# Kernel optimization log

Measured on AMD Instinct MI355X. Metric: run time of the kernel, lower is better.

## Reference

```python
import jax, jax.numpy as jnp
import numpy as np

N_NODES = 50000
N_EDGES = 800000
IN_DIM = 128
OUT_DIM = 128
N_CLASSES = 10
N_GRAPHS = 64


def setup_inputs() -> dict:
    key = jax.random.key(0)
    ks = jax.random.split(key, 8)
    features = jax.random.normal(ks[0], (N_NODES, IN_DIM), dtype=jnp.float32)
    src = jax.random.randint(ks[1], (N_EDGES,), 0, N_NODES, dtype=jnp.int64)
    dst = jax.random.randint(ks[2], (N_EDGES,), 0, N_NODES, dtype=jnp.int64)
    graph_ids = jnp.sort(jax.random.randint(ks[3], (N_NODES,), 0, N_GRAPHS, dtype=jnp.int64))
    # GraphConv params (glorot-ish scale) and linear head params
    W = jax.random.normal(ks[4], (IN_DIM, OUT_DIM), dtype=jnp.float32) / np.sqrt(IN_DIM)
    b = jnp.zeros((OUT_DIM,), dtype=jnp.float32)
    W_head = jax.random.normal(ks[5], (OUT_DIM, N_CLASSES), dtype=jnp.float32) / np.sqrt(OUT_DIM)
    b_head = jnp.zeros((N_CLASSES,), dtype=jnp.float32)
    return {"features": features, "src": src, "dst": dst, "graph_ids": graph_ids,
            "W": W, "b": b, "W_head": W_head, "b_head": b_head}


def reference(features, src, dst, graph_ids, W, b, W_head, b_head):
    # DGL GraphConv, norm='both': D_out^-1/2 -> sum aggregate -> D_in^-1/2 -> XW+b -> relu
    ones_e = jnp.ones((src.shape[0],), dtype=features.dtype)
    out_deg = jax.ops.segment_sum(ones_e, src, num_segments=N_NODES)
    in_deg = jax.ops.segment_sum(ones_e, dst, num_segments=N_NODES)
    out_norm = jax.lax.rsqrt(jnp.clip(out_deg, 1.0))[:, None]   # [N,1]
    in_norm = jax.lax.rsqrt(jnp.clip(in_deg, 1.0))[:, None]     # [N,1]
    h = features * out_norm                                      # [N,D]
    agg = jax.ops.segment_sum(h[src], dst, num_segments=N_NODES) # gather-scatter [E,D]->[N,D]
    agg = agg * in_norm
    h = jax.nn.relu(agg @ W + b)                                 # [N,D_out]
    # dgl.mean_nodes: segment mean over graphs (note: original returns after layer 0)
    cnt = jax.ops.segment_sum(jnp.ones((N_NODES,), dtype=h.dtype), graph_ids, num_segments=N_GRAPHS)
    pooled = jax.ops.segment_sum(h, graph_ids, num_segments=N_GRAPHS) / jnp.clip(cnt, 1.0)[:, None]
    return pooled @ W_head + b_head                              # [G, n_classes]
```

## Files before the change

kernel.cpp:

```cpp
#include <hip/hip_runtime.h>

#define N_NODES   50000
#define N_EDGES   800000
#define DIM       128
#define N_GRAPHS  64
#define N_CLASSES 10
#define NCHE      128
#define CSZ       (N_EDGES / NCHE)
#define LQ        (N_NODES / 4)
#define WPB       64
#define NBR2      ((LQ + WPB - 1) / WPB)
#define PLACE_BPC ((CSZ + 255) / 256)
#define PLACE_BLKS (NCHE * PLACE_BPC)
#define PRES_BLKS ((N_NODES * DIM / 8 + 255) / 256)
#define WT_BLKS   (DIM * DIM / 256)
#define NPBM      128
#define NBLK_NODE ((N_NODES + NPBM - 1) / NPBM)

typedef _Float16 h8 __attribute__((ext_vector_type(8)));
typedef float f4v __attribute__((ext_vector_type(4)));

__global__ __launch_bounds__(256) void k_lhist(const int* __restrict__ src,
                                               const int* __restrict__ dst,
                                               unsigned* __restrict__ Hin,
                                               unsigned* __restrict__ Hout,
                                               unsigned char* __restrict__ perm) {
    __shared__ unsigned L[LQ];
    int c = blockIdx.x, t = threadIdx.x;
    int base = c * CSZ;
    for (int w = t; w < LQ; w += 256) L[w] = 0u;
    __syncthreads();
    if (blockIdx.y == 0) {
        for (int i = t; i < CSZ; i += 256) {
            int d = dst[base + i];
            int sh = (d & 3) * 8;
            unsigned old = atomicAdd(&L[d >> 2], 1u << sh);
            perm[base + i] = (unsigned char)((old >> sh) & 0xffu);
        }
        __syncthreads();
        for (int w = t; w < LQ; w += 256) Hin[(size_t)c * LQ + w] = L[w];
    } else {
        for (int i = t; i < CSZ; i += 256) {
            int s = src[base + i];
            atomicAdd(&L[s >> 2], 1u << ((s & 3) * 8));
        }
        __syncthreads();
        for (int w = t; w < LQ; w += 256) Hout[(size_t)c * LQ + w] = L[w];
    }
}

__global__ __launch_bounds__(256) void k_reduce(unsigned* __restrict__ Hin,
                                                const unsigned* __restrict__ Hout,
                                                const int* __restrict__ gid,
                                                unsigned* __restrict__ indeg,
                                                float* __restrict__ outnorm,
                                                float* __restrict__ innorm,
                                                int* __restrict__ start,
                                                unsigned* __restrict__ row_ptr,
                                                unsigned* __restrict__ blockSums) {
    __shared__ unsigned sIn[4][WPB];
    __shared__ unsigned sOut[4][WPB];
    __shared__ unsigned sS[WPB];
    int t = threadIdx.x;
    int wl = t & (WPB - 1);
    int g  = t >> 6;
    int w  = blockIdx.x * WPB + wl;
    unsigned gs = 0, os = 0;
    int c0 = g * (NCHE / 4);
    if (w < LQ) {
        for (int c = c0; c < c0 + NCHE / 4; ++c) {
            gs += Hin[(size_t)c * LQ + w];
            os += Hout[(size_t)c * LQ + w];
        }
    }
    sIn[g][wl] = gs; sOut[g][wl] = os;
    __syncthreads();
    unsigned baseg = 0;
    for (int gg = 0; gg < 4; ++gg) if (gg < g) baseg += sIn[gg][wl];
    if (w < LQ) {
        unsigned running = baseg;
        for (int c = c0; c < c0 + NCHE / 4; ++c) {
            size_t idx = (size_t)c * LQ + w;
            unsigned word = Hin[idx];
            Hin[idx] = running;
            running += word;
        }
    }
    unsigned tot = 0, otot = 0, wtot = 0;
    if (t < WPB) {
        tot  = sIn[0][t] + sIn[1][t] + sIn[2][t] + sIn[3][t];
        otot = sOut[0][t] + sOut[1][t] + sOut[2][t] + sOut[3][t];
        wtot = (tot & 0xffu) + ((tot >> 8) & 0xffu) + ((tot >> 16) & 0xffu) + (tot >> 24);
        sS[t] = wtot;
    }
    __syncthreads();
    for (int off = 1; off < WPB; off <<= 1) {
        unsigned x = (t < WPB && t >= off) ? sS[t - off] : 0u;
        __syncthreads();
        if (t < WPB) sS[t] += x;
        __syncthreads();
    }
    if (t < WPB) {
        int ww = blockIdx.x * WPB + t;
        if (ww < LQ) {
            unsigned r0 = tot & 0xffu, r1 = (tot >> 8) & 0xffu,
                     r2 = (tot >> 16) & 0xffu, r3 = tot >> 24;
            unsigned o0 = otot & 0xffu, o1 = (otot >> 8) & 0xffu,
                     o2 = (otot >> 16) & 0xffu, o3 = otot >> 24;
            unsigned ex = sS[t] - wtot;
            int n = 4 * ww;
            row_ptr[n]     = ex;
            row_ptr[n + 1] = ex + r0;
            row_ptr[n + 2] = ex + r0 + r1;
            row_ptr[n + 3] = ex + r0 + r1 + r2;
            unsigned rr[4] = {r0, r1, r2, r3}, oo[4] = {o0, o1, o2, o3};
#pragma unroll
            for (int j = 0; j < 4; ++j) {
                indeg[n + j]   = rr[j];
                innorm[n + j]  = rsqrtf(fmaxf((float)rr[j], 1.0f));
                outnorm[n + j] = rsqrtf(fmaxf((float)oo[j], 1.0f));
                int i = n + j;
                int gq = gid[i];
                if (i == 0) {
                    for (int x2 = 0; x2 <= gq; ++x2) start[x2] = 0;
                } else {
                    int gp = gid[i - 1];
                    if (gp != gq)
                        for (int x2 = gp + 1; x2 <= gq; ++x2) start[x2] = i;
                }
                if (i == N_NODES - 1)
                    for (int x2 = gq + 1; x2 <= N_GRAPHS; ++x2) start[x2] = N_NODES;
            }
        }
        if (t == WPB - 1) blockSums[blockIdx.x] = sS[WPB - 1];
    }
}

__global__ __launch_bounds__(256) void k_scan2(unsigned* __restrict__ blockSums,
                                               unsigned* __restrict__ blockOff,
                                               float* __restrict__ pooled) {
    __shared__ unsigned s[256];
    int t = threadIdx.x;
    unsigned val = (t < NBR2) ? blockSums[t] : 0u;
    s[t] = val;
    __syncthreads();
    for (int off = 1; off < 256; off <<= 1) {
        unsigned x = (t >= off) ? s[t - off] : 0u;
        __syncthreads();
        s[t] += x;
        __syncthreads();
    }
    if (t < NBR2) blockOff[t] = s[t] - val;
    float4 z = {0.f, 0.f, 0.f, 0.f};
    for (int i = t; i < N_GRAPHS * DIM / 4; i += 256)
        reinterpret_cast<float4*>(pooled)[i] = z;
}

__global__ __launch_bounds__(256) void k_prep(const int* __restrict__ src,
                                              const int* __restrict__ dst,
                                              const unsigned* __restrict__ Hin,
                                              const unsigned char* __restrict__ perm,
                                              const unsigned* __restrict__ row_ptr,
                                              const unsigned* __restrict__ blockOff,
                                              int* __restrict__ bsrc,
                                              const float* __restrict__ feat,
                                              const float* __restrict__ outnorm,
                                              _Float16* __restrict__ sfeat,
                                              const float* __restrict__ W,
                                              _Float16* __restrict__ Wt) {
    int t = threadIdx.x;
    int blk = blockIdx.x;
    if (blk < PLACE_BLKS) {
        int c = blk / PLACE_BPC;
        int i = (blk % PLACE_BPC) * 256 + t;
        if (i < CSZ) {
            int e = c * CSZ + i;
            int d = dst[e];
            int sh = (d & 3) * 8;
            unsigned pre = (Hin[(size_t)c * LQ + (d >> 2)] >> sh) & 0xffu;
            unsigned pos = row_ptr[d] + blockOff[d >> 8] + pre + perm[e];
            bsrc[pos] = src[e];
        }
    } else if (blk < PLACE_BLKS + PRES_BLKS) {
        int i = (blk - PLACE_BLKS) * 256 + t;
        if (i < N_NODES * DIM / 8) {
            int n = i >> 4;
            int d = (i & 15) << 3;
            float nrm = outnorm[n];
            const float4* p = reinterpret_cast<const float4*>(feat + (size_t)n * DIM + d);
            float4 a = p[0], q = p[1];
            h8 r;
            r[0] = (_Float16)(a.x * nrm); r[1] = (_Float16)(a.y * nrm);
            r[2] = (_Float16)(a.z * nrm); r[3] = (_Float16)(a.w * nrm);
            r[4] = (_Float16)(q.x * nrm); r[5] = (_Float16)(q.y * nrm);
            r[6] = (_Float16)(q.z * nrm); r[7] = (_Float16)(q.w * nrm);
            *reinterpret_cast<h8*>(sfeat + (size_t)n * DIM + d) = r;
        }
    } else {
        int i = (blk - PLACE_BLKS - PRES_BLKS) * 256 + t;
        int n = i >> 7, k = i & 127;
        Wt[n * DIM + k] = (_Float16)W[k * DIM + n];
    }
}

#define CVT8(ACC_A, ACC_B, R, M) \
    ACC_A.x += (M) * (float)R[0]; ACC_A.y += (M) * (float)R[1]; \
    ACC_A.z += (M) * (float)R[2]; ACC_A.w += (M) * (float)R[3]; \
    ACC_B.x += (M) * (float)R[4]; ACC_B.y += (M) * (float)R[5]; \
    ACC_B.z += (M) * (float)R[6]; ACC_B.w += (M) * (float)R[7];

__global__ __launch_bounds__(256) void k_gather(const int* __restrict__ bsrc,
                                                const unsigned* __restrict__ row_ptr,
                                                const unsigned* __restrict__ blockOff,
                                                const unsigned* __restrict__ indeg,
                                                const _Float16* __restrict__ sfeat,
                                                const float* __restrict__ innorm,
                                                _Float16* __restrict__ aggh) {
    int tid = threadIdx.x;
    int wave = tid >> 6;
    int lane = tid & 63;
    int node = blockIdx.x * 4 + wave;
    if (node >= N_NODES) return;
    unsigned start = row_ptr[node] + blockOff[node >> 8];
    unsigned deg   = indeg[node];
    unsigned lim   = deg < 64u ? deg : 64u;
    int qtr = lane >> 4;
    int d8  = (lane & 15) << 3;
    int sIdx = 0;
    if ((unsigned)lane < lim) sIdx = bsrc[start + lane];
    float4 accA = {0,0,0,0}, accB = {0,0,0,0};
    float4 accC = {0,0,0,0}, accD = {0,0,0,0};
    for (unsigned j = 0; j < lim; j += 16) {
        unsigned j0 = j + qtr, j1 = j + 4 + qtr, j2 = j + 8 + qtr, j3 = j + 12 + qtr;
        int s0 = __shfl(sIdx, (int)(j0 < lim ? j0 : 0u));
        int s1 = __shfl(sIdx, (int)(j1 < lim ? j1 : 0u));
        int s2 = __shfl(sIdx, (int)(j2 < lim ? j2 : 0u));
        int s3 = __shfl(sIdx, (int)(j3 < lim ? j3 : 0u));
        float m0 = (j0 < lim) ? 1.f : 0.f;
        float m1 = (j1 < lim) ? 1.f : 0.f;
        float m2 = (j2 < lim) ? 1.f : 0.f;
        float m3 = (j3 < lim) ? 1.f : 0.f;
        h8 r0 = *reinterpret_cast<const h8*>(sfeat + (size_t)s0 * DIM + d8);
        h8 r1 = *reinterpret_cast<const h8*>(sfeat + (size_t)s1 * DIM + d8);
        h8 r2 = *reinterpret_cast<const h8*>(sfeat + (size_t)s2 * DIM + d8);
        h8 r3 = *reinterpret_cast<const h8*>(sfeat + (size_t)s3 * DIM + d8);
        CVT8(accA, accB, r0, m0);
        CVT8(accC, accD, r1, m1);
        CVT8(accA, accB, r2, m2);
        CVT8(accC, accD, r3, m3);
    }
    for (unsigned j = 64; j < deg; j += 4) {
        unsigned jj = j + qtr;
        bool valid = jj < deg;
        int s = bsrc[start + (valid ? jj : 0u)];
        float m = valid ? 1.f : 0.f;
        h8 r = *reinterpret_cast<const h8*>(sfeat + (size_t)s * DIM + d8);
        CVT8(accA, accB, r, m);
    }
    accA.x += accC.x; accA.y += accC.y; accA.z += accC.z; accA.w += accC.w;
    accB.x += accD.x; accB.y += accD.y; accB.z += accD.z; accB.w += accD.w;
    accA.x += __shfl_down(accA.x, 32); accA.y += __shfl_down(accA.y, 32);
    accA.z += __shfl_down(accA.z, 32); accA.w += __shfl_down(accA.w, 32);
    accB.x += __shfl_down(accB.x, 32); accB.y += __shfl_down(accB.y, 32);
    accB.z += __shfl_down(accB.z, 32); accB.w += __shfl_down(accB.w, 32);
    accA.x += __shfl_down(accA.x, 16); accA.y += __shfl_down(accA.y, 16);
    accA.z += __shfl_down(accA.z, 16); accA.w += __shfl_down(accA.w, 16);
    accB.x += __shfl_down(accB.x, 16); accB.y += __shfl_down(accB.y, 16);
    accB.z += __shfl_down(accB.z, 16); accB.w += __shfl_down(accB.w, 16);
    if (qtr == 0) {
        float innrm = innorm[node];
        h8 r;
        r[0] = (_Float16)(accA.x * innrm); r[1] = (_Float16)(accA.y * innrm);
        r[2] = (_Float16)(accA.z * innrm); r[3] = (_Float16)(accA.w * innrm);
        r[4] = (_Float16)(accB.x * innrm); r[5] = (_Float16)(accB.y * innrm);
        r[6] = (_Float16)(accB.z * innrm); r[7] = (_Float16)(accB.w * innrm);
        *reinterpret_cast<h8*>(aggh + (size_t)node * DIM + d8) = r;
    }
}

__global__ __launch_bounds__(256) void k_node(const _Float16* __restrict__ aggh,
                                              const int* __restrict__ gid,
                                              const _Float16* __restrict__ Wt,
                                              const float* __restrict__ b,
                                              float* __restrict__ pooled) {
    __shared__ float red[4][2][DIM];
    int tid = threadIdx.x;
    int wave = tid >> 6, lane = tid & 63;
    int quad = lane >> 4, m = lane & 15;
    int blockBase = blockIdx.x * NPBM;
    int wbase = blockBase + wave * 32;
    int gfirst = gid[blockBase];
    int gsec = gfirst + 1;

    f4v acc0[8], acc1[8];
#pragma unroll
    for (int t = 0; t < 8; ++t) { acc0[t] = (f4v){0,0,0,0}; acc1[t] = (f4v){0,0,0,0}; }

#pragma unroll
    for (int kk = 0; kk < 4; ++kk) {
        int ko = kk * 32 + quad * 8;
        h8 a0 = *reinterpret_cast<const h8*>(aggh + (size_t)(wbase + m) * DIM + ko);
        h8 a1 = *reinterpret_cast<const h8*>(aggh + (size_t)(wbase + 16 + m) * DIM + ko);
#pragma unroll
        for (int t = 0; t < 8; ++t) {
            h8 bf = *reinterpret_cast<const h8*>(Wt + (size_t)(t * 16 + m) * DIM + ko);
            acc0[t] = __builtin_amdgcn_mfma_f32_16x16x32_f16(a0, bf, acc0[t], 0, 0, 0);
            acc1[t] = __builtin_amdgcn_mfma_f32_16x16x32_f16(a1, bf, acc1[t], 0, 0, 0);
        }
    }

    int n0 = wbase + quad * 4;
    int n1 = n0 + 16;
    float s0[8], s1[8];
#pragma unroll
    for (int t = 0; t < 8; ++t) {
        float bb = b[t * 16 + m];
        s0[t] = 0.f; s1[t] = 0.f;
#pragma unroll
        for (int r = 0; r < 4; ++r) {
            int node = n0 + r;
            if (node < N_NODES) {
                float h = fmaxf(acc0[t][r] + bb, 0.f);
                int g = gid[node];
                if (g == gfirst)      s0[t] += h;
                else if (g == gsec)   s1[t] += h;
                else atomicAdd(&pooled[(size_t)g * DIM + t * 16 + m], h);
            }
            int node2 = n1 + r;
            if (node2 < N_NODES) {
                float h = fmaxf(acc1[t][r] + bb, 0.f);
                int g = gid[node2];
                if (g == gfirst)      s0[t] += h;
                else if (g == gsec)   s1[t] += h;
                else atomicAdd(&pooled[(size_t)g * DIM + t * 16 + m], h);
            }
        }
        s0[t] += __shfl_down(s0[t], 32);
        s0[t] += __shfl_down(s0[t], 16);
        s1[t] += __shfl_down(s1[t], 32);
        s1[t] += __shfl_down(s1[t], 16);
    }
    if (quad == 0) {
#pragma unroll
        for (int t = 0; t < 8; ++t) {
            red[wave][0][t * 16 + m] = s0[t];
            red[wave][1][t * 16 + m] = s1[t];
        }
    }
    __syncthreads();
    if (tid < DIM) {
        float v0 = red[0][0][tid] + red[1][0][tid] + red[2][0][tid] + red[3][0][tid];
        if (v0 != 0.f) atomicAdd(&pooled[(size_t)gfirst * DIM + tid], v0);
        float v1 = red[0][1][tid] + red[1][1][tid] + red[2][1][tid] + red[3][1][tid];
        if (v1 != 0.f && gsec < N_GRAPHS) atomicAdd(&pooled[(size_t)gsec * DIM + tid], v1);
    }
}

__global__ __launch_bounds__(256) void k_head(const float* __restrict__ pooled,
                                              const int* __restrict__ start,
                                              const float* __restrict__ Wh,
                                              const float* __restrict__ bh,
                                              float* __restrict__ out) {
    int i = blockIdx.x * 256 + threadIdx.x;
    if (i >= N_GRAPHS * N_CLASSES) return;
    int g = i / N_CLASSES, c = i % N_CLASSES;
    const float* pr = pooled + g * DIM;
    float s = 0.f;
#pragma unroll 8
    for (int k = 0; k < DIM; ++k) s += pr[k] * Wh[k * N_CLASSES + c];
    float cntf = fmaxf((float)(start[g + 1] - start[g]), 1.0f);
    out[i] = s / cntf + bh[c];
}

extern "C" void kernel_launch(void* const* d_in, const int* in_sizes, int n_in,
                              void* d_out, int out_size, void* d_ws, size_t ws_size,
                              hipStream_t stream) {
    const float* feat = (const float*)d_in[0];
    const int*   src  = (const int*)d_in[1];
    const int*   dst  = (const int*)d_in[2];
    const int*   gid  = (const int*)d_in[3];
    const float* W    = (const float*)d_in[4];
    const float* b    = (const float*)d_in[5];
    const float* Wh   = (const float*)d_in[6];
    const float* bh   = (const float*)d_in[7];
    float* out = (float*)d_out;

    float*    pooled   = (float*)d_ws;
    unsigned* indeg    = (unsigned*)(pooled + (size_t)N_GRAPHS * DIM);
    float*    outnorm  = (float*)(indeg + N_NODES);
    float*    innorm   = outnorm + N_NODES;
    int*      start    = (int*)(innorm + N_NODES);
    unsigned* row_ptr  = (unsigned*)(start + N_GRAPHS + 1);
    unsigned* blockSums= row_ptr + N_NODES;
    unsigned* blockOff = blockSums + 256;
    unsigned char* perm= (unsigned char*)(blockOff + 256);
    int*      bsrc     = (int*)(perm + N_EDGES);
    _Float16* sfeat    = (_Float16*)(bsrc + N_EDGES);
    _Float16* aggh     = sfeat + (size_t)N_NODES * DIM;
    _Float16* Wt       = aggh + (size_t)N_NODES * DIM;
    unsigned* Hin      = (unsigned*)(Wt + DIM * DIM);
    unsigned* Hout     = Hin + (size_t)NCHE * LQ;

    dim3 lh(NCHE, 2);
    k_lhist <<<lh, 256, 0, stream>>>(src, dst, Hin, Hout, perm);
    k_reduce<<<NBR2, 256, 0, stream>>>(Hin, Hout, gid, indeg, outnorm, innorm,
                                       start, row_ptr, blockSums);
    k_scan2 <<<1, 256, 0, stream>>>(blockSums, blockOff, pooled);
    k_prep  <<<PLACE_BLKS + PRES_BLKS + WT_BLKS, 256, 0, stream>>>(
                src, dst, Hin, perm, row_ptr, blockOff, bsrc,
                feat, outnorm, sfeat, W, Wt);
    k_gather<<<(N_NODES + 3) / 4, 256, 0, stream>>>(bsrc, row_ptr, blockOff, indeg,
                                                    sfeat, innorm, aggh);
    k_node  <<<NBLK_NODE, 256, 0, stream>>>(aggh, gid, Wt, b, pooled);
    k_head  <<<3, 256, 0, stream>>>(pooled, start, Wh, bh, out);
}
```

Measured before the change: 188.8 us.

## Split feature matrix into 32-column panels and gather per panel

Stores the normalized fp16 features and the aggregated output in four column panels of 32 halves (64 bytes) per node. The gather kernel gets a second grid dimension over panels, so each wave handles 16 edges at once on a 64-byte slice instead of 4 edges on full 256-byte rows. Each panel (about 3.2 MB) is meant to fit better in cache during the random gather. The cost is four times as many blocks, each reloading the CSR row pointers and edge indices, plus a longer shuffle reduction.

```diff
diff --git a/kernel.cpp b/kernel.cpp
--- a/kernel.cpp
+++ b/kernel.cpp
@@ -186,15 +186,16 @@
         if (i < N_NODES * DIM / 8) {
             int n = i >> 4;
             int d = (i & 15) << 3;
+            int p = d >> 5, off = d & 31;
             float nrm = outnorm[n];
-            const float4* p = reinterpret_cast<const float4*>(feat + (size_t)n * DIM + d);
-            float4 a = p[0], q = p[1];
+            const float4* pp = reinterpret_cast<const float4*>(feat + (size_t)n * DIM + d);
+            float4 a = pp[0], q = pp[1];
             h8 r;
             r[0] = (_Float16)(a.x * nrm); r[1] = (_Float16)(a.y * nrm);
             r[2] = (_Float16)(a.z * nrm); r[3] = (_Float16)(a.w * nrm);
             r[4] = (_Float16)(q.x * nrm); r[5] = (_Float16)(q.y * nrm);
             r[6] = (_Float16)(q.z * nrm); r[7] = (_Float16)(q.w * nrm);
-            *reinterpret_cast<h8*>(sfeat + (size_t)n * DIM + d) = r;
+            *reinterpret_cast<h8*>(sfeat + ((size_t)p * N_NODES + n) * 32 + off) = r;
         }
     } else {
         int i = (blk - PLACE_BLKS - PRES_BLKS) * 256 + t;
@@ -221,60 +222,53 @@
     int lane = tid & 63;
     int node = blockIdx.x * 4 + wave;
     if (node >= N_NODES) return;
+    int p = blockIdx.y;
+    const _Float16* sbase = sfeat + (size_t)p * N_NODES * 32;
     unsigned start = row_ptr[node] + blockOff[node >> 8];
     unsigned deg   = indeg[node];
     unsigned lim   = deg < 64u ? deg : 64u;
-    int qtr = lane >> 4;
-    int d8  = (lane & 15) << 3;
+    int slot = lane >> 2;
+    int d8   = (lane & 3) << 3;
     int sIdx = 0;
     if ((unsigned)lane < lim) sIdx = bsrc[start + lane];
     float4 accA = {0,0,0,0}, accB = {0,0,0,0};
     float4 accC = {0,0,0,0}, accD = {0,0,0,0};
-    for (unsigned j = 0; j < lim; j += 16) {
-        unsigned j0 = j + qtr, j1 = j + 4 + qtr, j2 = j + 8 + qtr, j3 = j + 12 + qtr;
+    for (unsigned j = 0; j < lim; j += 32) {
+        unsigned j0 = j + slot, j1 = j + 16 + slot;
         int s0 = __shfl(sIdx, (int)(j0 < lim ? j0 : 0u));
         int s1 = __shfl(sIdx, (int)(j1 < lim ? j1 : 0u));
-        int s2 = __shfl(sIdx, (int)(j2 < lim ? j2 : 0u));
-        int s3 = __shfl(sIdx, (int)(j3 < lim ? j3 : 0u));
         float m0 = (j0 < lim) ? 1.f : 0.f;
         float m1 = (j1 < lim) ? 1.f : 0.f;
-        float m2 = (j2 < lim) ? 1.f : 0.f;
-        float m3 = (j3 < lim) ? 1.f : 0.f;
-        h8 r0 = *reinterpret_cast<const h8*>(sfeat + (size_t)s0 * DIM + d8);
-        h8 r1 = *reinterpret_cast<const h8*>(sfeat + (size_t)s1 * DIM + d8);
-        h8 r2 = *reinterpret_cast<const h8*>(sfeat + (size_t)s2 * DIM + d8);
-        h8 r3 = *reinterpret_cast<const h8*>(sfeat + (size_t)s3 * DIM + d8);
+        h8 r0 = *reinterpret_cast<const h8*>(sbase + (size_t)s0 * 32 + d8);
+        h8 r1 = *reinterpret_cast<const h8*>(sbase + (size_t)s1 * 32 + d8);
         CVT8(accA, accB, r0, m0);
         CVT8(accC, accD, r1, m1);
-        CVT8(accA, accB, r2, m2);
-        CVT8(accC, accD, r3, m3);
-    }
-    for (unsigned j = 64; j < deg; j += 4) {
-        unsigned jj = j + qtr;
+    }
+    for (unsigned j = 64; j < deg; j += 16) {
+        unsigned jj = j + slot;
         bool valid = jj < deg;
         int s = bsrc[start + (valid ? jj : 0u)];
         float m = valid ? 1.f : 0.f;
-        h8 r = *reinterpret_cast<const h8*>(sfeat + (size_t)s * DIM + d8);
+        h8 r = *reinterpret_cast<const h8*>(sbase + (size_t)s * 32 + d8);
         CVT8(accA, accB, r, m);
     }
     accA.x += accC.x; accA.y += accC.y; accA.z += accC.z; accA.w += accC.w;
     accB.x += accD.x; accB.y += accD.y; accB.z += accD.z; accB.w += accD.w;
-    accA.x += __shfl_down(accA.x, 32); accA.y += __shfl_down(accA.y, 32);
-    accA.z += __shfl_down(accA.z, 32); accA.w += __shfl_down(accA.w, 32);
-    accB.x += __shfl_down(accB.x, 32); accB.y += __shfl_down(accB.y, 32);
-    accB.z += __shfl_down(accB.z, 32); accB.w += __shfl_down(accB.w, 32);
-    accA.x += __shfl_down(accA.x, 16); accA.y += __shfl_down(accA.y, 16);
-    accA.z += __shfl_down(accA.z, 16); accA.w += __shfl_down(accA.w, 16);
-    accB.x += __shfl_down(accB.x, 16); accB.y += __shfl_down(accB.y, 16);
-    accB.z += __shfl_down(accB.z, 16); accB.w += __shfl_down(accB.w, 16);
-    if (qtr == 0) {
+#pragma unroll
+    for (int off = 32; off >= 4; off >>= 1) {
+        accA.x += __shfl_down(accA.x, off); accA.y += __shfl_down(accA.y, off);
+        accA.z += __shfl_down(accA.z, off); accA.w += __shfl_down(accA.w, off);
+        accB.x += __shfl_down(accB.x, off); accB.y += __shfl_down(accB.y, off);
+        accB.z += __shfl_down(accB.z, off); accB.w += __shfl_down(accB.w, off);
+    }
+    if (slot == 0) {
         float innrm = innorm[node];
         h8 r;
         r[0] = (_Float16)(accA.x * innrm); r[1] = (_Float16)(accA.y * innrm);
         r[2] = (_Float16)(accA.z * innrm); r[3] = (_Float16)(accA.w * innrm);
         r[4] = (_Float16)(accB.x * innrm); r[5] = (_Float16)(accB.y * innrm);
         r[6] = (_Float16)(accB.z * innrm); r[7] = (_Float16)(accB.w * innrm);
-        *reinterpret_cast<h8*>(aggh + (size_t)node * DIM + d8) = r;
+        *reinterpret_cast<h8*>(aggh + ((size_t)p * N_NODES + node) * 32 + d8) = r;
     }
 }
 
@@ -299,8 +293,8 @@
 #pragma unroll
     for (int kk = 0; kk < 4; ++kk) {
         int ko = kk * 32 + quad * 8;
-        h8 a0 = *reinterpret_cast<const h8*>(aggh + (size_t)(wbase + m) * DIM + ko);
-        h8 a1 = *reinterpret_cast<const h8*>(aggh + (size_t)(wbase + 16 + m) * DIM + ko);
+        h8 a0 = *reinterpret_cast<const h8*>(aggh + ((size_t)kk * N_NODES + wbase + m) * 32 + quad * 8);
+        h8 a1 = *reinterpret_cast<const h8*>(aggh + ((size_t)kk * N_NODES + wbase + 16 + m) * 32 + quad * 8);
 #pragma unroll
         for (int t = 0; t < 8; ++t) {
             h8 bf = *reinterpret_cast<const h8*>(Wt + (size_t)(t * 16 + m) * DIM + ko);
@@ -409,8 +403,9 @@
     k_prep  <<<PLACE_BLKS + PRES_BLKS + WT_BLKS, 256, 0, stream>>>(
                 src, dst, Hin, perm, row_ptr, blockOff, bsrc,
                 feat, outnorm, sfeat, W, Wt);
-    k_gather<<<(N_NODES + 3) / 4, 256, 0, stream>>>(bsrc, row_ptr, blockOff, indeg,
-                                                    sfeat, innorm, aggh);
+    dim3 gg((N_NODES + 3) / 4, 4);
+    k_gather<<<gg, 256, 0, stream>>>(bsrc, row_ptr, blockOff, indeg,
+                                     sfeat, innorm, aggh);
     k_node  <<<NBLK_NODE, 256, 0, stream>>>(aggh, gid, Wt, b, pooled);
     k_head  <<<3, 256, 0, stream>>>(pooled, start, Wh, bh, out);
 }
```

New measurement: 224.3 us. 18.8% more time.
